# Performance work log

Hardware: AMD Instinct MI355X
Metric: run time of the kernel (lower is better)

The kernel has to match this reference:

```python
import jax, jax.numpy as jnp
import numpy as np

K = 3
TOPK = 32
TELEPORT = 0.1
LN_EPS = 1e-5


def _block(x, ln_g, ln_b, w1, b1, w2, b2, log_tau, gate):
    residual = x
    # pre: LayerNorm -> Linear -> GELU (exact erf, torch default)
    mu = jnp.mean(x, axis=-1, keepdims=True)
    var = jnp.mean(jnp.square(x - mu), axis=-1, keepdims=True)
    h = (x - mu) * jax.lax.rsqrt(var + LN_EPS) * ln_g + ln_b
    h = jax.nn.gelu(h @ w1 + b1, approximate=False)  # [B, N, H]

    # dynamic cosine adjacency with top-k sparsification
    tau = jnp.maximum(jnp.exp(log_tau), 1e-3)
    xn = h / jnp.maximum(jnp.linalg.norm(h, axis=-1, keepdims=True), 1e-12)
    A = jnp.maximum(jnp.einsum('bnf,bmf->bnm', xn, xn), 0.0)  # [B, N, N]
    B, N, _ = A.shape
    vals, idx = jax.lax.top_k(A, TOPK)  # idx: [B, N, TOPK]
    bi = jnp.arange(B)[:, None, None]
    ni = jnp.arange(N)[None, :, None]
    mask = jnp.zeros(A.shape, dtype=bool).at[bi, ni, idx].set(True)
    I = jnp.eye(N, dtype=A.dtype)
    A = jnp.where(mask, A, 0.0) + I
    A = A / tau

    # teleport + symmetric degree normalization
    A = (1.0 - TELEPORT) * A + TELEPORT * I
    deg = jnp.maximum(A.sum(-1), 1e-6)  # [B, N]
    dm12 = deg ** -0.5
    Ahat = dm12[:, :, None] * A * dm12[:, None, :]

    # Chebyshev propagation
    T0 = h
    outs = [T0]
    if K > 1:
        T1 = jnp.einsum('bnm,bmf->bnf', Ahat, T0)
        outs.append(T1)
    for _ in range(2, K):
        outs.append(2.0 * jnp.einsum('bnm,bmf->bnf', Ahat, outs[-1]) - outs[-2])
    hcat = jnp.concatenate(outs, axis=-1)  # [B, N, H*K]
    y = hcat @ w2 + b2
    return residual + jnp.tanh(gate) * y


def setup_inputs() -> dict:
    key = jax.random.key(0)
    k0, k1, k2 = jax.random.split(key, 3)
    Bsz, N, D, H, O = 4, 4096, 128, 128, 128
    x = jax.random.normal(k0, (Bsz, N, D), dtype=jnp.float32)
    ln_g = jnp.ones((D,), jnp.float32)
    ln_b = jnp.zeros((D,), jnp.float32)
    w1 = jax.random.normal(k1, (D, H), jnp.float32) / np.float32(np.sqrt(D))
    b1 = jnp.zeros((H,), jnp.float32)
    w2 = jax.random.normal(k2, (H * K, O), jnp.float32) / np.float32(np.sqrt(H * K))
    b2 = jnp.zeros((O,), jnp.float32)
    log_tau = jnp.asarray(np.log(0.5), jnp.float32)
    gate = jnp.asarray(0.2, jnp.float32)
    return {"x": x, "ln_g": ln_g, "ln_b": ln_b, "w1": w1, "b1": b1,
            "w2": w2, "b2": b2, "log_tau": log_tau, "gate": gate}


def reference(x, ln_g, ln_b, w1, b1, w2, b2, log_tau, gate):
    return _block(x, ln_g, ln_b, w1, b1, w2, b2, log_tau, gate)
```

## Files before the change

### kernel.cpp

```cpp
#include <hip/hip_runtime.h>
#include <hip/hip_bf16.h>
#include <stdint.h>

#define NB 4
#define NN 4096

using f16x8 = __attribute__((ext_vector_type(8))) _Float16;
using f32x4 = __attribute__((ext_vector_type(4))) float;

__device__ __forceinline__ float wave_sum(float v) {
  #pragma unroll
  for (int o = 32; o > 0; o >>= 1) v += __shfl_xor(v, o, 64);
  return v;
}
__device__ __forceinline__ float h2f_bits(unsigned hb) {
  unsigned short us = (unsigned short)hb;
  _Float16 hf;
  __builtin_memcpy(&hf, &us, 2);
  return (float)hf;
}
__device__ __forceinline__ unsigned short f2h_bits(float f) {
  _Float16 hf = (_Float16)f;
  unsigned short us;
  __builtin_memcpy(&us, &hf, 2);
  return us;
}
__device__ __forceinline__ unsigned pack2h(float lo, float hi) {
  return ((unsigned)f2h_bits(hi) << 16) | (unsigned)f2h_bits(lo);
}

#define INS16(c) do { unsigned t_;                      \
  t_ = max(l0, c);  c = min(l0, c);  l0 = t_;           \
  t_ = max(l1, c);  c = min(l1, c);  l1 = t_;           \
  t_ = max(l2, c);  c = min(l2, c);  l2 = t_;           \
  t_ = max(l3, c);  c = min(l3, c);  l3 = t_;           \
  t_ = max(l4, c);  c = min(l4, c);  l4 = t_;           \
  t_ = max(l5, c);  c = min(l5, c);  l5 = t_;           \
  t_ = max(l6, c);  c = min(l6, c);  l6 = t_;           \
  t_ = max(l7, c);  c = min(l7, c);  l7 = t_;           \
  t_ = max(l8, c);  c = min(l8, c);  l8 = t_;           \
  t_ = max(l9, c);  c = min(l9, c);  l9 = t_;           \
  t_ = max(l10, c); c = min(l10, c); l10 = t_;          \
  t_ = max(l11, c); c = min(l11, c); l11 = t_;          \
  t_ = max(l12, c); c = min(l12, c); l12 = t_;          \
  t_ = max(l13, c); c = min(l13, c); l13 = t_;          \
  t_ = max(l14, c); c = min(l14, c); l14 = t_;          \
  l15 = max(l15, c);                                    \
} while (0)

__global__ __launch_bounds__(128) void k_prep(const float* __restrict__ w1,
                                              _Float16* __restrict__ w1t16) {
  int n = blockIdx.x;
  int k = threadIdx.x;
  __shared__ _Float16 v16[128];
  v16[k] = (_Float16)w1[(size_t)k * 128 + n];
  __syncthreads();
  if (k < 16) {
    union { _Float16 hh[8]; uint4 u; } pk;
    #pragma unroll
    for (int j = 0; j < 8; ++j) pk.hh[j] = v16[k * 8 + j];
    *(uint4*)(w1t16 + (size_t)n * 128 + (size_t)(k ^ (n & 7)) * 8) = pk.u;
  }
}

__global__ __launch_bounds__(128) void k_prep2(const float* __restrict__ w2,
                                               _Float16* __restrict__ w2t16) {
  int n = blockIdx.x;
  int t = threadIdx.x;
  __shared__ float v[384];
  #pragma unroll
  for (int i = 0; i < 3; ++i) v[i * 128 + t] = w2[(size_t)(i * 128 + t) * 128 + n];
  __syncthreads();
  if (t < 48) {
    int kc = t >> 4, cl = t & 15;
    union { _Float16 hh[8]; uint4 u; } pk;
    #pragma unroll
    for (int e = 0; e < 8; ++e) pk.hh[e] = (_Float16)v[t * 8 + e];
    *(uint4*)(w2t16 + (size_t)n * 384 + kc * 128 + (size_t)(cl ^ (n & 7)) * 8) = pk.u;
  }
}

__global__ __launch_bounds__(256) void k0_ln(
    const float* __restrict__ x, const float* __restrict__ ln_g,
    const float* __restrict__ ln_b, _Float16* __restrict__ ln16) {
  int lane = threadIdx.x & 63;
  int row = blockIdx.x * 4 + (threadIdx.x >> 6);
  float2 xv = ((const float2*)x)[(size_t)row * 64 + lane];
  float2 gv = ((const float2*)ln_g)[lane];
  float2 bv = ((const float2*)ln_b)[lane];
  float mu = wave_sum(xv.x + xv.y) * (1.0f / 128.0f);
  float dx = xv.x - mu, dy = xv.y - mu;
  float var = wave_sum(dx * dx + dy * dy) * (1.0f / 128.0f);
  float ri = 1.0f / sqrtf(var + 1e-5f);
  float h0 = dx * ri * gv.x + bv.x;
  float h1 = dy * ri * gv.y + bv.y;
  int c = lane >> 2;
  int addr = row * 128 + ((c ^ (row & 7)) << 3) + (lane & 3) * 2;
  *(unsigned*)(ln16 + addr) = pack2h(h0, h1);
}

__global__ __launch_bounds__(256) void k1_mfma(
    const _Float16* __restrict__ ln16, const _Float16* __restrict__ w1t16,
    const float* __restrict__ b1, _Float16* __restrict__ h16,
    _Float16* __restrict__ hn16) {
  __shared__ _Float16 As[64 * 128];
  __shared__ _Float16 Bs[128 * 128];
  int tid = threadIdx.x;
  int lane = tid & 63;
  int wv = tid >> 6;
  int rbase = blockIdx.x * 64;
  #pragma unroll
  for (int i = 0; i < 4; ++i) {
    int idx = tid + 256 * i;
    __builtin_amdgcn_global_load_lds(
        (const __attribute__((address_space(1))) void*)(ln16 + (size_t)rbase * 128 + (size_t)idx * 8),
        (__attribute__((address_space(3))) void*)(As + (size_t)idx * 8), 16, 0, 0);
  }
  #pragma unroll
  for (int i = 0; i < 8; ++i) {
    int idx = tid + 256 * i;
    __builtin_amdgcn_global_load_lds(
        (const __attribute__((address_space(1))) void*)(w1t16 + (size_t)idx * 8),
        (__attribute__((address_space(3))) void*)(Bs + (size_t)idx * 8), 16, 0, 0);
  }
  asm volatile("s_waitcnt vmcnt(0)" ::: "memory");
  __syncthreads();

  int rl = lane & 15, kg = lane >> 4;
  f32x4 acc[8];
  #pragma unroll
  for (int j = 0; j < 8; ++j) acc[j] = (f32x4){0.f, 0.f, 0.f, 0.f};
  #pragma unroll
  for (int kk = 0; kk < 4; ++kk) {
    int cL = kk * 4 + kg;
    int r = wv * 16 + rl;
    f16x8 a = *(const f16x8*)(As + r * 128 + (cL ^ (r & 7)) * 8);
    #pragma unroll
    for (int j = 0; j < 8; ++j) {
      int n = j * 16 + rl;
      f16x8 bf = *(const f16x8*)(Bs + n * 128 + (cL ^ (n & 7)) * 8);
      acc[j] = __builtin_amdgcn_mfma_f32_16x16x32_f16(a, bf, acc[j], 0, 0, 0);
    }
  }
  float ssq[4] = {0.f, 0.f, 0.f, 0.f};
  #pragma unroll
  for (int j = 0; j < 8; ++j) {
    float bv = b1[j * 16 + rl];
    #pragma unroll
    for (int rg = 0; rg < 4; ++rg) {
      float z = acc[j][rg] + bv;
      float g = 0.5f * z * (1.0f + erff(z * 0.70710678118654752440f));
      acc[j][rg] = g;
      ssq[rg] += g * g;
    }
  }
  #pragma unroll
  for (int o = 1; o < 16; o <<= 1)
    #pragma unroll
    for (int rg = 0; rg < 4; ++rg) ssq[rg] += __shfl_xor(ssq[rg], o, 64);
  float rinv[4];
  #pragma unroll
  for (int rg = 0; rg < 4; ++rg) rinv[rg] = 1.0f / fmaxf(sqrtf(ssq[rg]), 1e-12f);

  #pragma unroll
  for (int j = 0; j < 8; ++j) {
    #pragma unroll
    for (int rg = 0; rg < 4; ++rg) {
      float g = acc[j][rg];
      float gp = __shfl_xor(g, 1, 64);
      if ((rl & 1) == 0) {
        int row = rbase + wv * 16 + kg * 4 + rg;
        int col = j * 16 + rl;
        int c = col >> 3;
        int ad = row * 128 + (((c ^ (row & 7))) << 3) + (col & 7);
        *(unsigned*)(h16 + ad) = pack2h(g, gp);
        *(unsigned*)(hn16 + ad) = pack2h(g * rinv[rg], gp * rinv[rg]);
      }
    }
  }
}

__global__ __launch_bounds__(256, 1) void k_scores_topk(
    const _Float16* __restrict__ hn16, int* __restrict__ nidx,
    float* __restrict__ nval, float* __restrict__ dm12,
    const float* __restrict__ p_log_tau) {
  __shared__ _Float16 Qs[64 * 128];
  __shared__ _Float16 Cs[2][128 * 128];
  __shared__ unsigned stk[32 * 256];
  int tid = threadIdx.x;
  int lane = tid & 63;
  int wv = tid >> 6;
  int rl = lane & 15, kg = lane >> 4;
  int blk = blockIdx.x;
  int b = blk >> 6;
  int qbase = (blk & 63) * 64;
  const _Float16* hb = hn16 + (size_t)b * NN * 128;

  #pragma unroll
  for (int i = 0; i < 4; ++i) {
    int idx = tid + 256 * i;
    __builtin_amdgcn_global_load_lds(
        (const __attribute__((address_space(1))) void*)(hb + (size_t)qbase * 128 + (size_t)idx * 8),
        (__attribute__((address_space(3))) void*)(Qs + (size_t)idx * 8), 16, 0, 0);
  }
  #pragma unroll
  for (int i = 0; i < 8; ++i) {
    int idx = tid + 256 * i;
    __builtin_amdgcn_global_load_lds(
        (const __attribute__((address_space(1))) void*)(hb + (size_t)idx * 8),
        (__attribute__((address_space(3))) void*)(Cs[0] + (size_t)idx * 8), 16, 0, 0);
  }
  asm volatile("s_waitcnt vmcnt(0)" ::: "memory");
  __syncthreads();

  int qrow = wv * 16 + rl;
  f16x8 bq[4];
  #pragma unroll
  for (int kk = 0; kk < 4; ++kk)
    bq[kk] = *(const f16x8*)(Qs + qrow * 128 + ((kk * 4 + kg) ^ (qrow & 7)) * 8);

  unsigned l0 = 0, l1 = 0, l2 = 0, l3 = 0, l4 = 0, l5 = 0, l6 = 0, l7 = 0,
           l8 = 0, l9 = 0, l10 = 0, l11 = 0, l12 = 0, l13 = 0, l14 = 0, l15 = 0;

  for (int cb = 0; cb < 32; ++cb) {
    int cur = cb & 1;
    if (cb < 31) {
      const _Float16* csrc = hb + (size_t)(cb + 1) * 128 * 128;
      #pragma unroll
      for (int i = 0; i < 8; ++i) {
        int idx = tid + 256 * i;
        __builtin_amdgcn_global_load_lds(
            (const __attribute__((address_space(1))) void*)(csrc + (size_t)idx * 8),
            (__attribute__((address_space(3))) void*)(Cs[cur ^ 1] + (size_t)idx * 8), 16, 0, 0);
      }
    }
    f32x4 acc[8];
    #pragma unroll
    for (int j = 0; j < 8; ++j) acc[j] = (f32x4){0.f, 0.f, 0.f, 0.f};
    #pragma unroll
    for (int kk = 0; kk < 4; ++kk) {
      #pragma unroll
      for (int j = 0; j < 8; ++j) {
        int mrow = j * 16 + rl;
        f16x8 a = *(const f16x8*)(Cs[cur] + mrow * 128 + ((kk * 4 + kg) ^ (rl & 7)) * 8);
        acc[j] = __builtin_amdgcn_mfma_f32_16x16x32_f16(a, bq[kk], acc[j], 0, 0, 0);
      }
    }
    int cnt = 0;
    int mbase = cb * 128 + kg * 4;
    #pragma unroll
    for (int j = 0; j < 8; ++j) {
      #pragma unroll
      for (int rg = 0; rg < 4; ++rg) {
        float v = fmaxf(acc[j][rg], 0.0f);
        int m = mbase + j * 16 + rg;
        unsigned key = ((unsigned)f2h_bits(v) << 16) | (unsigned)(4095 - m);
        if (key > l15) {
          stk[cnt * 256 + tid] = key;
          ++cnt;
        }
      }
    }
    for (int i = 0;; ++i) {
      if (__ballot(i < cnt) == 0ull) break;
      unsigned c = (i < cnt) ? stk[i * 256 + tid] : 0u;
      INS16(c);
    }
    asm volatile("s_waitcnt vmcnt(0)" ::: "memory");
    __syncthreads();
  }

  unsigned sv[8];
  float sum = 0.0f;
  #pragma unroll
  for (int e = 0; e < 32; ++e) {
    unsigned v = l0;
    v = max(v, (unsigned)__shfl_xor((int)v, 16, 64));
    v = max(v, (unsigned)__shfl_xor((int)v, 32, 64));
    if (l0 == v) {
      l0 = l1; l1 = l2; l2 = l3; l3 = l4; l4 = l5; l5 = l6; l6 = l7; l7 = l8;
      l8 = l9; l9 = l10; l10 = l11; l11 = l12; l12 = l13; l13 = l14; l14 = l15; l15 = 0;
    }
    sum += h2f_bits(v >> 16);
    if (kg == (e & 3)) sv[e >> 2] = v;
  }
  int grow = b * NN + qbase + qrow;
  #pragma unroll
  for (int s = 0; s < 8; ++s) {
    unsigned v = sv[s];
    nidx[(size_t)grow * 32 + s * 4 + kg] = 4095 - (int)(v & 0xFFFu);
    nval[(size_t)grow * 32 + s * 4 + kg] = h2f_bits(v >> 16);
  }
  if (kg == 0) {
    float tau = fmaxf(expf(p_log_tau[0]), 1e-3f);
    float deg = fmaxf(0.9f * ((sum + 1.0f) / tau) + 0.1f, 1e-6f);
    dm12[grow] = 1.0f / sqrtf(deg);
  }
}

__global__ __launch_bounds__(128) void k_cheb1(
    const _Float16* __restrict__ h16, const int* __restrict__ nidx,
    const float* __restrict__ nval, const float* __restrict__ dm12,
    const float* __restrict__ p_log_tau, _Float16* __restrict__ T116) {
  int row = blockIdx.x;
  int b = row >> 12;
  int tid = threadIdx.x;
  __shared__ float cj[32];
  __shared__ int mj[32];
  __shared__ float cdsh;
  float tau = fmaxf(expf(p_log_tau[0]), 1e-3f);
  float scale = 0.9f / tau;
  float dn = dm12[row];
  if (tid < 32) {
    int m = nidx[(size_t)row * 32 + tid];
    cj[tid] = scale * nval[(size_t)row * 32 + tid] * dn * dm12[b * NN + m];
    mj[tid] = m;
  }
  if (tid == 0) cdsh = (scale + 0.1f) * dn * dn;
  __syncthreads();
  int c = tid >> 3, e = tid & 7;
  const _Float16* hb = h16 + (size_t)b * NN * 128;
  float acc = cdsh * (float)h16[(size_t)row * 128 + ((c ^ (row & 7)) << 3) + e];
  #pragma unroll 8
  for (int j = 0; j < 32; ++j) {
    int m = mj[j];
    acc += cj[j] * (float)hb[(size_t)m * 128 + ((c ^ (m & 7)) << 3) + e];
  }
  float p = __shfl_xor(acc, 1, 64);
  if (!(tid & 1))
    *(unsigned*)(T116 + (size_t)row * 128 + ((c ^ (row & 7)) << 3) + e) = pack2h(acc, p);
}

__global__ __launch_bounds__(128) void k_cheb2(
    const _Float16* __restrict__ h16, const _Float16* __restrict__ T116,
    const int* __restrict__ nidx, const float* __restrict__ nval,
    const float* __restrict__ dm12, const float* __restrict__ p_log_tau,
    _Float16* __restrict__ T216) {
  int row = blockIdx.x;
  int b = row >> 12;
  int tid = threadIdx.x;
  __shared__ float cj[32];
  __shared__ int mj[32];
  __shared__ float cdsh;
  float tau = fmaxf(expf(p_log_tau[0]), 1e-3f);
  float scale = 0.9f / tau;
  float dn = dm12[row];
  if (tid < 32) {
    int m = nidx[(size_t)row * 32 + tid];
    cj[tid] = scale * nval[(size_t)row * 32 + tid] * dn * dm12[b * NN + m];
    mj[tid] = m;
  }
  if (tid == 0) cdsh = (scale + 0.1f) * dn * dn;
  __syncthreads();
  int c = tid >> 3, e = tid & 7;
  int sw_own = ((c ^ (row & 7)) << 3) + e;
  const _Float16* T1b = T116 + (size_t)b * NN * 128;
  float a = cdsh * (float)T116[(size_t)row * 128 + sw_own];
  #pragma unroll 8
  for (int j = 0; j < 32; ++j) {
    int m = mj[j];
    a += cj[j] * (float)T1b[(size_t)m * 128 + ((c ^ (m & 7)) << 3) + e];
  }
  float t2 = 2.0f * a - (float)h16[(size_t)row * 128 + sw_own];
  float p = __shfl_xor(t2, 1, 64);
  if (!(tid & 1))
    *(unsigned*)(T216 + (size_t)row * 128 + sw_own) = pack2h(t2, p);
}

__global__ __launch_bounds__(256, 1) void k_out(
    const float* __restrict__ x, const _Float16* __restrict__ h16,
    const _Float16* __restrict__ T116, const _Float16* __restrict__ T216,
    const _Float16* __restrict__ w2t16, const float* __restrict__ b2,
    const float* __restrict__ p_gate, float* __restrict__ out) {
  __shared__ _Float16 As3[3][64 * 128];
  __shared__ _Float16 Bs3[3][128 * 128];
  int tid = threadIdx.x;
  int lane = tid & 63;
  int wv = tid >> 6;
  int rbase = blockIdx.x * 64;
  const _Float16* srcs[3] = {h16, T116, T216};
  #pragma unroll
  for (int kc = 0; kc < 3; ++kc) {
    const _Float16* src = srcs[kc] + (size_t)rbase * 128;
    #pragma unroll
    for (int i = 0; i < 4; ++i) {
      int idx = tid + 256 * i;
      __builtin_amdgcn_global_load_lds(
          (const __attribute__((address_space(1))) void*)(src + (size_t)idx * 8),
          (__attribute__((address_space(3))) void*)(As3[kc] + (size_t)idx * 8), 16, 0, 0);
    }
    #pragma unroll
    for (int i = 0; i < 8; ++i) {
      int idx = tid + 256 * i;
      int n = idx >> 4, cp = idx & 15;
      __builtin_amdgcn_global_load_lds(
          (const __attribute__((address_space(1))) void*)(w2t16 + (size_t)n * 384 + kc * 128 + (size_t)cp * 8),
          (__attribute__((address_space(3))) void*)(Bs3[kc] + (size_t)idx * 8), 16, 0, 0);
    }
  }
  asm volatile("s_waitcnt vmcnt(0)" ::: "memory");
  __syncthreads();

  int rl = lane & 15, kg = lane >> 4;
  f32x4 acc[8];
  #pragma unroll
  for (int j = 0; j < 8; ++j) acc[j] = (f32x4){0.f, 0.f, 0.f, 0.f};
  #pragma unroll
  for (int kc = 0; kc < 3; ++kc) {
    #pragma unroll
    for (int kk = 0; kk < 4; ++kk) {
      int cL = kk * 4 + kg;
      int r = wv * 16 + rl;
      f16x8 a = *(const f16x8*)(As3[kc] + r * 128 + (cL ^ (r & 7)) * 8);
      #pragma unroll
      for (int j = 0; j < 8; ++j) {
        int n = j * 16 + rl;
        f16x8 bf = *(const f16x8*)(Bs3[kc] + n * 128 + (cL ^ (n & 7)) * 8);
        acc[j] = __builtin_amdgcn_mfma_f32_16x16x32_f16(a, bf, acc[j], 0, 0, 0);
      }
    }
  }
  float tg = tanhf(p_gate[0]);
  #pragma unroll
  for (int j = 0; j < 8; ++j) {
    int col = j * 16 + rl;
    float bv = b2[col];
    #pragma unroll
    for (int rg = 0; rg < 4; ++rg) {
      int row = rbase + wv * 16 + kg * 4 + rg;
      out[(size_t)row * 128 + col] =
          x[(size_t)row * 128 + col] + tg * (acc[j][rg] + bv);
    }
  }
}

extern "C" void kernel_launch(void* const* d_in, const int* in_sizes, int n_in,
                              void* d_out, int out_size, void* d_ws, size_t ws_size,
                              hipStream_t stream) {
  (void)in_sizes; (void)n_in; (void)out_size; (void)ws_size;
  const float* x = (const float*)d_in[0];
  const float* ln_g = (const float*)d_in[1];
  const float* ln_b = (const float*)d_in[2];
  const float* w1 = (const float*)d_in[3];
  const float* b1 = (const float*)d_in[4];
  const float* w2 = (const float*)d_in[5];
  const float* b2 = (const float*)d_in[6];
  const float* p_log_tau = (const float*)d_in[7];
  const float* p_gate = (const float*)d_in[8];
  float* out = (float*)d_out;

  char* ws = (char*)d_ws;
  size_t off = 0;
  auto alloc = [&](size_t bytes) -> void* {
    off = (off + 255) & ~(size_t)255;
    void* p = ws + off;
    off += bytes;
    return p;
  };
  _Float16* ln16 = (_Float16*)alloc((size_t)NB * NN * 128 * 2);
  _Float16* h16 = (_Float16*)alloc((size_t)NB * NN * 128 * 2);
  _Float16* hn16 = (_Float16*)alloc((size_t)NB * NN * 128 * 2);
  _Float16* T116 = (_Float16*)alloc((size_t)NB * NN * 128 * 2);
  _Float16* T216 = (_Float16*)alloc((size_t)NB * NN * 128 * 2);
  _Float16* w1t16 = (_Float16*)alloc((size_t)128 * 128 * 2);
  _Float16* w2t16 = (_Float16*)alloc((size_t)128 * 384 * 2);
  int* nidx = (int*)alloc((size_t)NB * NN * 32 * 4);
  float* nval = (float*)alloc((size_t)NB * NN * 32 * 4);
  float* dm12 = (float*)alloc((size_t)NB * NN * 4);

  k_prep<<<128, 128, 0, stream>>>(w1, w1t16);
  k_prep2<<<128, 128, 0, stream>>>(w2, w2t16);
  k0_ln<<<NB * NN / 4, 256, 0, stream>>>(x, ln_g, ln_b, ln16);
  k1_mfma<<<NB * NN / 64, 256, 0, stream>>>(ln16, w1t16, b1, h16, hn16);
  k_scores_topk<<<NB * (NN / 64), 256, 0, stream>>>(hn16, nidx, nval, dm12, p_log_tau);
  k_cheb1<<<NB * NN, 128, 0, stream>>>(h16, nidx, nval, dm12, p_log_tau, T116);
  k_cheb2<<<NB * NN, 128, 0, stream>>>(h16, T116, nidx, nval, dm12, p_log_tau, T216);
  k_out<<<NB * NN / 64, 256, 0, stream>>>(x, h16, T116, T216, w2t16, b2, p_gate, out);
}
```

Before: 191.4 us.

## Split top-k scoring across column slices and merge partial lists in new kernel

The fused score+top-k kernel now splits the 4096 candidate columns into four slices, so four times as many blocks run, each with smaller LDS tiles and two blocks per CU allowed. Each block writes per-lane partial top-16 lists to a workspace, and a new merge kernel reduces the 256 candidates per row to the final top-32 plus the degree normalisation. The insertion filter now uses a float threshold derived from the current 16th-best key. This adds an extra kernel launch and a 16 MB intermediate buffer in exchange for better GPU occupancy on the dominant kernel.

```diff
diff --git a/kernel.cpp b/kernel.cpp
--- a/kernel.cpp
+++ b/kernel.cpp
@@ -180,34 +180,31 @@
   }
 }
 
-__global__ __launch_bounds__(256, 1) void k_scores_topk(
-    const _Float16* __restrict__ hn16, int* __restrict__ nidx,
-    float* __restrict__ nval, float* __restrict__ dm12,
-    const float* __restrict__ p_log_tau) {
+__global__ __launch_bounds__(256, 2) void k_scores_topk(
+    const _Float16* __restrict__ hn16, unsigned* __restrict__ pnk) {
   __shared__ _Float16 Qs[64 * 128];
-  __shared__ _Float16 Cs[2][128 * 128];
-  __shared__ unsigned stk[32 * 256];
+  __shared__ _Float16 Cs[2][64 * 128];
+  __shared__ unsigned stk[16 * 256];
   int tid = threadIdx.x;
   int lane = tid & 63;
   int wv = tid >> 6;
   int rl = lane & 15, kg = lane >> 4;
   int blk = blockIdx.x;
-  int b = blk >> 6;
-  int qbase = (blk & 63) * 64;
+  int b = blk >> 8;
+  int qb = (blk >> 2) & 63;
+  int sl = blk & 3;
+  int qbase = qb * 64;
+  int msl = sl * 1024;
   const _Float16* hb = hn16 + (size_t)b * NN * 128;
 
   #pragma unroll
   for (int i = 0; i < 4; ++i) {
     int idx = tid + 256 * i;
     __builtin_amdgcn_global_load_lds(
-        (const __attribute__((address_space(1))) void*)(hb + (size_t)qbase * 128 + (size_t)idx * 8),
+        (const __attribute__((address_space(1))) void*)(hb + (size_t)(qbase)*128 + (size_t)idx * 8),
         (__attribute__((address_space(3))) void*)(Qs + (size_t)idx * 8), 16, 0, 0);
-  }
-  #pragma unroll
-  for (int i = 0; i < 8; ++i) {
-    int idx = tid + 256 * i;
     __builtin_amdgcn_global_load_lds(
-        (const __attribute__((address_space(1))) void*)(hb + (size_t)idx * 8),
+        (const __attribute__((address_space(1))) void*)(hb + (size_t)msl * 128 + (size_t)idx * 8),
         (__attribute__((address_space(3))) void*)(Cs[0] + (size_t)idx * 8), 16, 0, 0);
   }
   asm volatile("s_waitcnt vmcnt(0)" ::: "memory");
@@ -221,41 +218,42 @@
 
   unsigned l0 = 0, l1 = 0, l2 = 0, l3 = 0, l4 = 0, l5 = 0, l6 = 0, l7 = 0,
            l8 = 0, l9 = 0, l10 = 0, l11 = 0, l12 = 0, l13 = 0, l14 = 0, l15 = 0;
-
-  for (int cb = 0; cb < 32; ++cb) {
+  float thresh = 0.0f;
+
+  for (int cb = 0; cb < 16; ++cb) {
     int cur = cb & 1;
-    if (cb < 31) {
-      const _Float16* csrc = hb + (size_t)(cb + 1) * 128 * 128;
+    if (cb < 15) {
+      const _Float16* csrc = hb + (size_t)(msl + (cb + 1) * 64) * 128;
       #pragma unroll
-      for (int i = 0; i < 8; ++i) {
+      for (int i = 0; i < 4; ++i) {
         int idx = tid + 256 * i;
         __builtin_amdgcn_global_load_lds(
             (const __attribute__((address_space(1))) void*)(csrc + (size_t)idx * 8),
             (__attribute__((address_space(3))) void*)(Cs[cur ^ 1] + (size_t)idx * 8), 16, 0, 0);
       }
     }
-    f32x4 acc[8];
-    #pragma unroll
-    for (int j = 0; j < 8; ++j) acc[j] = (f32x4){0.f, 0.f, 0.f, 0.f};
+    f32x4 acc[4];
+    #pragma unroll
+    for (int j = 0; j < 4; ++j) acc[j] = (f32x4){0.f, 0.f, 0.f, 0.f};
     #pragma unroll
     for (int kk = 0; kk < 4; ++kk) {
       #pragma unroll
-      for (int j = 0; j < 8; ++j) {
+      for (int j = 0; j < 4; ++j) {
         int mrow = j * 16 + rl;
         f16x8 a = *(const f16x8*)(Cs[cur] + mrow * 128 + ((kk * 4 + kg) ^ (rl & 7)) * 8);
         acc[j] = __builtin_amdgcn_mfma_f32_16x16x32_f16(a, bq[kk], acc[j], 0, 0, 0);
       }
     }
     int cnt = 0;
-    int mbase = cb * 128 + kg * 4;
-    #pragma unroll
-    for (int j = 0; j < 8; ++j) {
+    int mbase = msl + cb * 64 + kg * 4;
+    #pragma unroll
+    for (int j = 0; j < 4; ++j) {
       #pragma unroll
       for (int rg = 0; rg < 4; ++rg) {
         float v = fmaxf(acc[j][rg], 0.0f);
-        int m = mbase + j * 16 + rg;
-        unsigned key = ((unsigned)f2h_bits(v) << 16) | (unsigned)(4095 - m);
-        if (key > l15) {
+        if (v >= thresh) {
+          int m = mbase + j * 16 + rg;
+          unsigned key = ((unsigned)f2h_bits(v) << 16) | (unsigned)(4095 - m);
           stk[cnt * 256 + tid] = key;
           ++cnt;
         }
@@ -266,35 +264,50 @@
       unsigned c = (i < cnt) ? stk[i * 256 + tid] : 0u;
       INS16(c);
     }
+    unsigned hb16 = l15 >> 16;
+    thresh = (hb16 > 0) ? h2f_bits(hb16 - 1) : 0.0f;
     asm volatile("s_waitcnt vmcnt(0)" ::: "memory");
     __syncthreads();
   }
 
-  unsigned sv[8];
+  int grow = b * NN + qbase + qrow;
+  unsigned* dst = pnk + (size_t)grow * 256 + sl * 64 + kg * 16;
+  *(uint4*)(dst + 0)  = (uint4){l0, l1, l2, l3};
+  *(uint4*)(dst + 4)  = (uint4){l4, l5, l6, l7};
+  *(uint4*)(dst + 8)  = (uint4){l8, l9, l10, l11};
+  *(uint4*)(dst + 12) = (uint4){l12, l13, l14, l15};
+}
+
+__global__ __launch_bounds__(256) void k_topk_merge(
+    const unsigned* __restrict__ pnk, int* __restrict__ nidx,
+    float* __restrict__ nval, float* __restrict__ dm12,
+    const float* __restrict__ p_log_tau) {
+  int lane = threadIdx.x & 63;
+  int q = blockIdx.x * 4 + (threadIdx.x >> 6);
+  uint4 c4 = *(const uint4*)(pnk + (size_t)q * 256 + lane * 4);
+  unsigned k0 = c4.x, k1 = c4.y, k2 = c4.z, k3 = c4.w;
   float sum = 0.0f;
+  unsigned myv = 0;
   #pragma unroll
   for (int e = 0; e < 32; ++e) {
-    unsigned v = l0;
-    v = max(v, (unsigned)__shfl_xor((int)v, 16, 64));
-    v = max(v, (unsigned)__shfl_xor((int)v, 32, 64));
-    if (l0 == v) {
-      l0 = l1; l1 = l2; l2 = l3; l3 = l4; l4 = l5; l5 = l6; l6 = l7; l7 = l8;
-      l8 = l9; l9 = l10; l10 = l11; l11 = l12; l12 = l13; l13 = l14; l14 = l15; l15 = 0;
-    }
+    unsigned v = k0;
+    #pragma unroll
+    for (int o = 32; o > 0; o >>= 1) {
+      unsigned w = (unsigned)__shfl_xor((int)v, o, 64);
+      v = max(v, w);
+    }
+    if (k0 == v) { k0 = k1; k1 = k2; k2 = k3; k3 = 0; }
     sum += h2f_bits(v >> 16);
-    if (kg == (e & 3)) sv[e >> 2] = v;
-  }
-  int grow = b * NN + qbase + qrow;
-  #pragma unroll
-  for (int s = 0; s < 8; ++s) {
-    unsigned v = sv[s];
-    nidx[(size_t)grow * 32 + s * 4 + kg] = 4095 - (int)(v & 0xFFFu);
-    nval[(size_t)grow * 32 + s * 4 + kg] = h2f_bits(v >> 16);
-  }
-  if (kg == 0) {
+    if (lane == e) myv = v;
+  }
+  if (lane < 32) {
+    nidx[(size_t)q * 32 + lane] = 4095 - (int)(myv & 0xFFFu);
+    nval[(size_t)q * 32 + lane] = h2f_bits(myv >> 16);
+  }
+  if (lane == 0) {
     float tau = fmaxf(expf(p_log_tau[0]), 1e-3f);
     float deg = fmaxf(0.9f * ((sum + 1.0f) / tau) + 0.1f, 1e-6f);
-    dm12[grow] = 1.0f / sqrtf(deg);
+    dm12[q] = 1.0f / sqrtf(deg);
   }
 }
 
@@ -467,12 +480,14 @@
   int* nidx = (int*)alloc((size_t)NB * NN * 32 * 4);
   float* nval = (float*)alloc((size_t)NB * NN * 32 * 4);
   float* dm12 = (float*)alloc((size_t)NB * NN * 4);
+  unsigned* pnk = (unsigned*)alloc((size_t)NB * NN * 256 * 4);
 
   k_prep<<<128, 128, 0, stream>>>(w1, w1t16);
   k_prep2<<<128, 128, 0, stream>>>(w2, w2t16);
   k0_ln<<<NB * NN / 4, 256, 0, stream>>>(x, ln_g, ln_b, ln16);
   k1_mfma<<<NB * NN / 64, 256, 0, stream>>>(ln16, w1t16, b1, h16, hn16);
-  k_scores_topk<<<NB * (NN / 64), 256, 0, stream>>>(hn16, nidx, nval, dm12, p_log_tau);
+  k_scores_topk<<<NB * 256, 256, 0, stream>>>(hn16, pnk);
+  k_topk_merge<<<NB * NN / 4, 256, 0, stream>>>(pnk, nidx, nval, dm12, p_log_tau);
   k_cheb1<<<NB * NN, 128, 0, stream>>>(h16, nidx, nval, dm12, p_log_tau, T116);
   k_cheb2<<<NB * NN, 128, 0, stream>>>(h16, T116, nidx, nval, dm12, p_log_tau, T216);
   k_out<<<NB * NN / 64, 256, 0, stream>>>(x, h16, T116, T216, w2t16, b2, p_gate, out);
```

Result: slower. 214.5 us (+12.1%).
